# Kernel tuning notes

Hardware: AMD Instinct MI355X
Metric: run time of the kernel (lower is better)

Reference implementation:

```python
import jax, jax.numpy as jnp
import numpy as np

B, N, D, H = 8, 1025, 768, 12
PRE = 1            # prefix (CLS) tokens
P = N - PRE        # patch tokens
HD = D // H
EPS = 1e-6


def setup_inputs() -> dict:
    key = jax.random.key(0)
    ks = jax.random.split(key, 8)
    x = jax.random.normal(ks[0], (B, N, D), dtype=jnp.float32)
    graph = jax.random.uniform(ks[1], (B, P, P), dtype=jnp.float32)
    transferability = jax.random.uniform(ks[2], (B, P), dtype=jnp.float32)
    Wqkv = jax.random.normal(ks[3], (3 * D, D), dtype=jnp.float32) * 0.02
    bqkv = jnp.zeros((3 * D,), dtype=jnp.float32)
    Wproj = jax.random.normal(ks[4], (D, D), dtype=jnp.float32) * 0.02
    bproj = jnp.zeros((D,), dtype=jnp.float32)
    return {"x": x, "graph": graph, "transferability": transferability,
            "Wqkv": Wqkv, "bqkv": bqkv, "Wproj": Wproj, "bproj": bproj,
            "prefix_tokens": PRE}


def _build_mask(graph, transferability, prefix_tokens, n_tokens):
    # patch_weights: [B, P]
    pw = transferability / (jnp.sum(transferability, axis=1, keepdims=True) + EPS)
    b, p = pw.shape
    pre = prefix_tokens
    # Block layout: [[1s (pre,pre), pw broadcast (pre,P)], [pw[:,None] (P,pre), graph]]
    top_left = jnp.ones((b, pre, pre), dtype=graph.dtype)
    top_right = jnp.broadcast_to(pw[:, None, :], (b, pre, p))
    bot_left = jnp.broadcast_to(pw[:, :, None], (b, p, pre))
    top = jnp.concatenate([top_left, top_right], axis=2)
    bot = jnp.concatenate([bot_left, graph], axis=2)
    return jnp.concatenate([top, bot], axis=1)  # [B, N, N]


def reference(x, graph, transferability, Wqkv, bqkv, Wproj, bproj, prefix_tokens):
    bsz, n, d = x.shape
    scale = HD ** -0.5
    qkv = x @ Wqkv.T + bqkv                          # [B, N, 3D]
    qkv = qkv.reshape(bsz, n, 3, H, HD).transpose(2, 0, 3, 1, 4)  # [3, B, H, N, hd]
    q, k, v = qkv[0], qkv[1], qkv[2]
    attn = jax.nn.softmax(jnp.einsum('bhid,bhjd->bhij', q, k) * scale, axis=-1)
    mask = _build_mask(graph, transferability, prefix_tokens, n)  # [B, N, N]
    attn = attn * mask[:, None, :, :]
    attn = attn / (jnp.sum(attn, axis=-1, keepdims=True) + EPS)
    out = jnp.einsum('bhij,bhjd->bhid', attn, v)     # [B, H, N, hd]
    out = out.transpose(0, 2, 1, 3).reshape(bsz, n, d)
    return out @ Wproj.T + bproj
```

## Files before the change

kernel.cpp:

```cpp
#include <hip/hip_runtime.h>
#include <stdint.h>

constexpr int Bq = 8, Nn = 1025, Dd = 768, Hh = 12, HDd = 64, Pp = 1024;
constexpr int NP = 1088;
constexpr int MROWS = Bq * Nn;
constexpr float EPSI = 1e-6f;

typedef __attribute__((ext_vector_type(8))) short bfrag;
typedef __attribute__((ext_vector_type(4))) float ffrag;
typedef __attribute__((ext_vector_type(4))) float f4;
typedef __attribute__((ext_vector_type(4))) unsigned short us4;

#define MFMA16(a, b, c) __builtin_amdgcn_mfma_f32_16x16x32_bf16((a), (b), (c), 0, 0, 0)

#if __has_builtin(__builtin_amdgcn_exp2f)
#define EXP2(x) __builtin_amdgcn_exp2f(x)
#else
#define EXP2(x) exp2f(x)
#endif

__device__ __forceinline__ unsigned short f2bf(float f) {
  union { float f; uint32_t u; } v{f};
  uint32_t u = v.u;
  return (unsigned short)((u + 0x7fffu + ((u >> 16) & 1u)) >> 16);
}
__device__ __forceinline__ float bf2f(unsigned short s) {
  union { uint32_t u; float f; } v; v.u = ((uint32_t)s) << 16; return v.f;
}
__device__ __forceinline__ uint32_t pkbf(float a, float b) {
  uint32_t r;
  asm("v_cvt_pk_bf16_f32 %0, %1, %2" : "=v"(r) : "v"(a), "v"(b));
  return r;
}

__device__ __forceinline__ void gload16(const void* g, void* l) {
  __builtin_amdgcn_global_load_lds((const __attribute__((address_space(1))) unsigned int*)g,
                                   (__attribute__((address_space(3))) unsigned int*)l, 16, 0, 0);
}

__global__ __launch_bounds__(256) void conv3_kernel(const float* __restrict__ s0, unsigned short* __restrict__ d0, int n0,
                                                    const float* __restrict__ s1, unsigned short* __restrict__ d1, int n1,
                                                    const float* __restrict__ s2, unsigned short* __restrict__ d2, int n2) {
  int idx = blockIdx.x * blockDim.x + threadIdx.x;
  int stride = gridDim.x * blockDim.x;
  int ntot = n0 + n1 + n2;
  for (int i = idx; i < ntot; i += stride) {
    const float* src; unsigned short* dst; int k;
    if (i < n0) { src = s0; dst = d0; k = i; }
    else if (i < n0 + n1) { src = s1; dst = d1; k = i - n0; }
    else { src = s2; dst = d2; k = i - n0 - n1; }
    f4 v = ((const f4*)src)[k];
    us4 o; o[0] = f2bf(v[0]); o[1] = f2bf(v[1]); o[2] = f2bf(v[2]); o[3] = f2bf(v[3]);
    ((us4*)dst)[k] = o;
  }
}

__global__ __launch_bounds__(256) void pw_kernel(const float* __restrict__ tr, float* __restrict__ pw) {
  int b = blockIdx.x;
  __shared__ float red[256];
  float s = 0.f;
  for (int j = threadIdx.x; j < Pp; j += 256) s += tr[b * Pp + j];
  red[threadIdx.x] = s; __syncthreads();
  for (int o = 128; o > 0; o >>= 1) { if (threadIdx.x < o) red[threadIdx.x] += red[threadIdx.x + o]; __syncthreads(); }
  float inv = 1.f / (red[0] + EPSI);
  for (int j = threadIdx.x; j < Pp; j += 256) pw[b * Pp + j] = tr[b * Pp + j] * inv;
}

__global__ __launch_bounds__(256) void mask_kernel(const float* __restrict__ graph,
                                                   const float* __restrict__ pw,
                                                   unsigned short* __restrict__ mask) {
  int i = blockIdx.x, b = blockIdx.y;
  unsigned short* mrow = mask + ((size_t)b * NP + i) * NP;
  if (i >= Nn) { for (int j = threadIdx.x; j < NP; j += 256) mrow[j] = 0; return; }
  if (i == 0) {
    for (int j = threadIdx.x; j < NP; j += 256) {
      float v = (j == 0) ? 1.f : (j <= Pp ? pw[b * Pp + j - 1] : 0.f);
      mrow[j] = f2bf(v);
    }
  } else {
    const float* grow = graph + ((size_t)b * Pp + (i - 1)) * Pp;
    for (int j = threadIdx.x; j < NP; j += 256) {
      float v = (j == 0) ? pw[b * Pp + i - 1] : (j <= Pp ? grow[j - 1] : 0.f);
      mrow[j] = f2bf(v);
    }
  }
}

__global__ __launch_bounds__(256) void padzero_kernel(unsigned short* __restrict__ Qo,
                                                      unsigned short* __restrict__ Ko,
                                                      unsigned short* __restrict__ Vo) {
  int bh = blockIdx.x;
  unsigned short* qp = Qo + ((size_t)bh * NP + Nn) * 64;
  unsigned short* kp = Ko + ((size_t)bh * NP + Nn) * 64;
  for (int idx = threadIdx.x; idx < (NP - Nn) * 64; idx += 256) { qp[idx] = 0; kp[idx] = 0; }
  unsigned short* vp = Vo + (size_t)bh * 64 * NP;
  for (int idx = threadIdx.x; idx < 64 * (NP - Nn); idx += 256) {
    int d = idx / (NP - Nn), j = Nn + (idx - d * (NP - Nn));
    vp[(size_t)d * NP + j] = 0;
  }
}

__device__ __forceinline__ void gemm_main(const unsigned short* __restrict__ A, int rowA0, int rowAmax,
                                          const unsigned short* __restrict__ Bw, int rowB0,
                                          uint4* lds, ffrag acc[4][4], int tid) {
  const int l = tid & 63, lm = l & 15, lg = l >> 4, w = tid >> 6, wr = w >> 1, wc = w & 1;
  const unsigned short* aS[4]; const unsigned short* bS[4];
#pragma unroll
  for (int q = 0; q < 4; q++) {
    int c = tid + 256 * q, r = c >> 3, p = c & 7, g = p ^ (r & 7);
    int ra = rowA0 + r; if (ra > rowAmax) ra = rowAmax;
    aS[q] = A + (size_t)ra * 768 + 8 * g;
    bS[q] = Bw + (size_t)(rowB0 + r) * 768 + 8 * g;
  }
  uint4* buf0 = lds;
  uint4* buf1 = lds + 2048;
#pragma unroll
  for (int q = 0; q < 4; q++) {
    gload16(aS[q], buf0 + tid + 256 * q);
    gload16(bS[q], buf0 + 1024 + tid + 256 * q);
    aS[q] += 64; bS[q] += 64;
  }
  asm volatile("s_waitcnt vmcnt(0)" ::: "memory");
  __builtin_amdgcn_sched_barrier(0);
  __builtin_amdgcn_s_barrier();
#pragma unroll 1
  for (int kt = 0; kt < 12; kt++) {
    uint4* cur = (kt & 1) ? buf1 : buf0;
    uint4* nxt = (kt & 1) ? buf0 : buf1;
    if (kt < 11) {
#pragma unroll
      for (int q = 0; q < 4; q++) {
        gload16(aS[q], nxt + tid + 256 * q);
        gload16(bS[q], nxt + 1024 + tid + 256 * q);
        aS[q] += 64; bS[q] += 64;
      }
    }
    const bfrag* LA = (const bfrag*)cur;
    const bfrag* LB = (const bfrag*)(cur + 1024);
    bfrag af[4][2], bf_[4][2];
#pragma unroll
    for (int am = 0; am < 4; am++) {
      int row = wr * 64 + am * 16 + lm;
      af[am][0] = LA[row * 8 + ((0 + lg) ^ (row & 7))];
      af[am][1] = LA[row * 8 + ((4 + lg) ^ (row & 7))];
    }
#pragma unroll
    for (int an = 0; an < 4; an++) {
      int row = wc * 64 + an * 16 + lm;
      bf_[an][0] = LB[row * 8 + ((0 + lg) ^ (row & 7))];
      bf_[an][1] = LB[row * 8 + ((4 + lg) ^ (row & 7))];
    }
#pragma unroll
    for (int am = 0; am < 4; am++)
#pragma unroll
      for (int an = 0; an < 4; an++) {
        acc[am][an] = MFMA16(af[am][0], bf_[an][0], acc[am][an]);
        acc[am][an] = MFMA16(af[am][1], bf_[an][1], acc[am][an]);
      }
    asm volatile("s_waitcnt vmcnt(0)" ::: "memory");
    __builtin_amdgcn_sched_barrier(0);
    __builtin_amdgcn_s_barrier();
  }
}

__device__ __forceinline__ int xcd_chunk_map(int orig, int nwg) {
  int qq = nwg >> 3, rr = nwg & 7;
  int xcd = orig & 7, idx = orig >> 3;
  int base = (xcd < rr) ? xcd * (qq + 1) : rr * (qq + 1) + (xcd - rr) * qq;
  return base + idx;
}

__global__ __launch_bounds__(256) void qkv_gemm_kernel(const unsigned short* __restrict__ X,
                                                       const unsigned short* __restrict__ W,
                                                       const float* __restrict__ bias,
                                                       unsigned short* __restrict__ Qo,
                                                       unsigned short* __restrict__ Ko,
                                                       unsigned short* __restrict__ Vo) {
  __shared__ uint4 lds[4096];
  int tid = threadIdx.x;
  int wg = xcd_chunk_map(blockIdx.x, 65 * 18);
  int xt = wg / 18, yt = wg - 18 * xt;
  ffrag zero4 = {0.f, 0.f, 0.f, 0.f};
  ffrag acc[4][4];
#pragma unroll
  for (int i = 0; i < 4; i++)
#pragma unroll
    for (int j = 0; j < 4; j++) acc[i][j] = zero4;
  gemm_main(X, xt * 128, MROWS - 1, W, yt * 128, lds, acc, tid);
  const int l = tid & 63, lm = l & 15, lg = l >> 4, w = tid >> 6, wr = w >> 1, wc = w & 1;
#pragma unroll
  for (int an = 0; an < 4; an++) {
    int gc = yt * 128 + wc * 64 + an * 16 + lm;
    int which = gc / 768, rr = gc - which * 768, h = rr >> 6, hd = rr & 63;
    float bv = bias[gc];
#pragma unroll
    for (int am = 0; am < 4; am++) {
      int grb = xt * 128 + wr * 64 + am * 16 + 4 * lg;
#pragma unroll
      for (int r = 0; r < 4; r++) {
        int gr = grb + r;
        if (gr >= MROWS) continue;
        int b = gr / Nn, i = gr - b * Nn;
        size_t bh = (size_t)(b * Hh + h);
        float v = acc[am][an][r] + bv;
        if (which == 0)      Qo[(bh * NP + i) * 64 + hd] = f2bf(v * 0.18033688f);
        else if (which == 1) Ko[(bh * NP + i) * 64 + hd] = f2bf(v);
        else                 Vo[(bh * 64 + hd) * NP + i] = f2bf(v);
      }
    }
  }
}

__global__ __launch_bounds__(256) void proj_gemm_kernel(const unsigned short* __restrict__ A,
                                                        const unsigned short* __restrict__ W,
                                                        const float* __restrict__ bias,
                                                        float* __restrict__ out) {
  __shared__ uint4 lds[4096];
  int tid = threadIdx.x;
  int wg = xcd_chunk_map(blockIdx.x, 65 * 6);
  int xt = wg / 6, yt = wg - 6 * xt;
  ffrag zero4 = {0.f, 0.f, 0.f, 0.f};
  ffrag acc[4][4];
#pragma unroll
  for (int i = 0; i < 4; i++)
#pragma unroll
    for (int j = 0; j < 4; j++) acc[i][j] = zero4;
  gemm_main(A, xt * 128, MROWS - 1, W, yt * 128, lds, acc, tid);
  const int l = tid & 63, lm = l & 15, lg = l >> 4, w = tid >> 6, wr = w >> 1, wc = w & 1;
#pragma unroll
  for (int an = 0; an < 4; an++) {
    int gc = yt * 128 + wc * 64 + an * 16 + lm;
    float bv = bias[gc];
#pragma unroll
    for (int am = 0; am < 4; am++) {
      int grb = xt * 128 + wr * 64 + am * 16 + 4 * lg;
#pragma unroll
      for (int r = 0; r < 4; r++) {
        int gr = grb + r;
        if (gr >= MROWS) continue;
        out[(size_t)gr * 768 + gc] = acc[am][an][r] + bv;
      }
    }
  }
}

__global__ __launch_bounds__(256) void attn_kernel(const unsigned short* __restrict__ Qg,
                                                   const unsigned short* __restrict__ Kg,
                                                   const unsigned short* __restrict__ Vg,
                                                   const unsigned short* __restrict__ Mg,
                                                   unsigned short* __restrict__ Og) {
  __shared__ uint4 smem[3072];
  int tid = threadIdx.x, w = tid >> 6, l = tid & 63, lm = l & 15, lg = l >> 4;
  int bx = blockIdx.x;
  int b = bx & 7, t5 = bx >> 3;
  int h = t5 % 12, ib = t5 / 12;
  size_t bh = (size_t)(b * Hh + h);
  const unsigned short* Qb = Qg + bh * NP * 64;
  const unsigned short* Kb = Kg + bh * NP * 64;
  const unsigned short* Vb = Vg + bh * 64 * NP;
  int i0a = ib * 128 + w * 16;
  int i0b = i0a + 64;
  int irowa = i0a + lm; if (irowa > NP - 1) irowa = NP - 1;
  int irowb = i0b + lm; if (irowb > NP - 1) irowb = NP - 1;
  const unsigned short* Mrowa = Mg + (size_t)b * NP * NP + (size_t)irowa * NP;
  const unsigned short* Mrowb = Mg + (size_t)b * NP * NP + (size_t)irowb * NP;

  bfrag qa0 = *(const bfrag*)(Qb + (size_t)irowa * 64 + 8 * lg);
  bfrag qa1 = *(const bfrag*)(Qb + (size_t)irowa * 64 + 32 + 8 * lg);
  bfrag qb0 = *(const bfrag*)(Qb + (size_t)irowb * 64 + 8 * lg);
  bfrag qb1 = *(const bfrag*)(Qb + (size_t)irowb * 64 + 32 + 8 * lg);

  ffrag zero4 = {0.f, 0.f, 0.f, 0.f};
  ffrag oaccA[4] = {zero4, zero4, zero4, zero4};
  ffrag oaccB[4] = {zero4, zero4, zero4, zero4};
  float TpA = 0.f, TpB = 0.f;

  int rS = tid >> 3, pS = tid & 7;
  int rS2 = rS + 32;
  const unsigned short* kS0 = Kb + (size_t)rS * 64 + 8 * (pS ^ (rS & 7));
  const unsigned short* kS1 = Kb + (size_t)rS2 * 64 + 8 * (pS ^ (rS2 & 7));
  const unsigned short* vS0 = Vb + (size_t)rS * NP + 8 * (pS ^ (rS & 7));
  const unsigned short* vS1 = Vb + (size_t)rS2 * NP + 8 * (pS ^ (rS2 & 7));

  char* PAbase = (char*)(smem + 2048) + w * 4096;
  char* PBbase = PAbase + 2048;

  gload16(kS0, smem + tid);
  gload16(kS1, smem + tid + 256);
  gload16(vS0, smem + 512 + tid);
  gload16(vS1, smem + 512 + tid + 256);
  asm volatile("s_waitcnt vmcnt(0)" ::: "memory");
  __builtin_amdgcn_sched_barrier(0);
  __builtin_amdgcn_s_barrier();

#pragma unroll 1
  for (int t = 0; t < 17; t++) {
    int cb = (t & 1) << 10;
    if (t < 16) {
      int nb = ((t + 1) & 1) << 10;
      size_t ko = (size_t)(t + 1) * 4096;
      int vo = (t + 1) * 64;
      gload16(kS0 + ko, smem + nb + tid);
      gload16(kS1 + ko, smem + nb + tid + 256);
      gload16(vS0 + vo, smem + nb + 512 + tid);
      gload16(vS1 + vo, smem + nb + 512 + tid + 256);
    }
    int j0 = t * 64;
    us4 mvA[4], mvB[4];
#pragma unroll
    for (int jm = 0; jm < 4; jm++) {
      mvA[jm] = *(const us4*)(Mrowa + j0 + 16 * jm + 4 * lg);
      mvB[jm] = *(const us4*)(Mrowb + j0 + 16 * jm + 4 * lg);
    }
    const bfrag* LK = (const bfrag*)(smem + cb);
    const bfrag* LV = (const bfrag*)(smem + cb + 512);

    bfrag ka[4], kb2[4];
#pragma unroll
    for (int jm = 0; jm < 4; jm++) {
      int row = jm * 16 + lm;
      ka[jm]  = LK[row * 8 + ((0 + lg) ^ (row & 7))];
      kb2[jm] = LK[row * 8 + ((4 + lg) ^ (row & 7))];
    }
    ffrag sa[4], sb[4];
    __builtin_amdgcn_s_setprio(1);
#pragma unroll
    for (int jm = 0; jm < 4; jm++) {
      ffrag a = zero4;
      a = MFMA16(ka[jm], qa0, a);
      a = MFMA16(kb2[jm], qa1, a);
      sa[jm] = a;
      ffrag bb = zero4;
      bb = MFMA16(ka[jm], qb0, bb);
      bb = MFMA16(kb2[jm], qb1, bb);
      sb[jm] = bb;
    }
    __builtin_amdgcn_s_setprio(0);

    bfrag vf[2][4];
#pragma unroll
    for (int ks = 0; ks < 2; ks++)
#pragma unroll
      for (int dm = 0; dm < 4; dm++) {
        int vrow = dm * 16 + lm;
        vf[ks][dm] = LV[vrow * 8 + ((ks * 4 + lg) ^ (vrow & 7))];
      }

#pragma unroll
    for (int jm = 0; jm < 4; jm++) {
      float p0 = EXP2(sa[jm][0]), p1 = EXP2(sa[jm][1]), p2 = EXP2(sa[jm][2]), p3 = EXP2(sa[jm][3]);
      float q0 = p0 * bf2f(mvA[jm][0]), q1 = p1 * bf2f(mvA[jm][1]);
      float q2 = p2 * bf2f(mvA[jm][2]), q3 = p3 * bf2f(mvA[jm][3]);
      TpA += (q0 + q1) + (q2 + q3);
      uint2 pk; pk.x = pkbf(q0, q1); pk.y = pkbf(q2, q3);
      int cpos = (((jm << 1) | (lg >> 1)) ^ (lm & 7));
      *(uint2*)(PAbase + lm * 128 + cpos * 16 + 8 * (lg & 1)) = pk;
    }
#pragma unroll
    for (int jm = 0; jm < 4; jm++) {
      float p0 = EXP2(sb[jm][0]), p1 = EXP2(sb[jm][1]), p2 = EXP2(sb[jm][2]), p3 = EXP2(sb[jm][3]);
      float q0 = p0 * bf2f(mvB[jm][0]), q1 = p1 * bf2f(mvB[jm][1]);
      float q2 = p2 * bf2f(mvB[jm][2]), q3 = p3 * bf2f(mvB[jm][3]);
      TpB += (q0 + q1) + (q2 + q3);
      uint2 pk; pk.x = pkbf(q0, q1); pk.y = pkbf(q2, q3);
      int cpos = (((jm << 1) | (lg >> 1)) ^ (lm & 7));
      *(uint2*)(PBbase + lm * 128 + cpos * 16 + 8 * (lg & 1)) = pk;
    }
    __builtin_amdgcn_s_setprio(1);
#pragma unroll
    for (int ks = 0; ks < 2; ks++) {
      bfrag pa = *(const bfrag*)(PAbase + lm * 128 + ((((ks << 2) | lg)) ^ (lm & 7)) * 16);
#pragma unroll
      for (int dm = 0; dm < 4; dm++) oaccA[dm] = MFMA16(pa, vf[ks][dm], oaccA[dm]);
    }
#pragma unroll
    for (int ks = 0; ks < 2; ks++) {
      bfrag pb = *(const bfrag*)(PBbase + lm * 128 + ((((ks << 2) | lg)) ^ (lm & 7)) * 16);
#pragma unroll
      for (int dm = 0; dm < 4; dm++) oaccB[dm] = MFMA16(pb, vf[ks][dm], oaccB[dm]);
    }
    __builtin_amdgcn_s_setprio(0);

    asm volatile("s_waitcnt vmcnt(0)" ::: "memory");
    __builtin_amdgcn_sched_barrier(0);
    __builtin_amdgcn_s_barrier();
  }
  TpA += __shfl_xor(TpA, 16); TpA += __shfl_xor(TpA, 32);
  TpB += __shfl_xor(TpB, 16); TpB += __shfl_xor(TpB, 32);
  float dnA_row = 1.f / TpA;
  float dnB_row = 1.f / TpB;
  float dnA[4], dnB[4];
#pragma unroll
  for (int r = 0; r < 4; r++) { dnA[r] = __shfl(dnA_row, 4 * lg + r); dnB[r] = __shfl(dnB_row, 4 * lg + r); }
#pragma unroll
  for (int dm = 0; dm < 4; dm++)
#pragma unroll
    for (int r = 0; r < 4; r++) {
      int ia = i0a + 4 * lg + r;
      if (ia < Nn) Og[((size_t)(b * Nn + ia)) * Dd + h * 64 + dm * 16 + lm] = f2bf(oaccA[dm][r] * dnA[r]);
      int ibr = i0b + 4 * lg + r;
      if (ibr < Nn) Og[((size_t)(b * Nn + ibr)) * Dd + h * 64 + dm * 16 + lm] = f2bf(oaccB[dm][r] * dnB[r]);
    }
}

extern "C" void kernel_launch(void* const* d_in, const int* in_sizes, int n_in,
                              void* d_out, int out_size, void* d_ws, size_t ws_size,
                              hipStream_t stream) {
  const float* x      = (const float*)d_in[0];
  const float* graph  = (const float*)d_in[1];
  const float* transf = (const float*)d_in[2];
  const float* Wqkv   = (const float*)d_in[3];
  const float* bqkv   = (const float*)d_in[4];
  const float* Wproj  = (const float*)d_in[5];
  const float* bproj  = (const float*)d_in[6];
  float* out = (float*)d_out;
  char* ws = (char*)d_ws;

  unsigned short* xbf  = (unsigned short*)(ws + 0);
  unsigned short* wqb  = (unsigned short*)(ws + 12595200);
  unsigned short* wpb  = (unsigned short*)(ws + 16134144);
  unsigned short* Qb   = (unsigned short*)(ws + 17313792);
  unsigned short* Kb   = (unsigned short*)(ws + 30683136);
  unsigned short* Vb   = (unsigned short*)(ws + 44052480);
  float*          pw   = (float*)(ws + 57421824);
  unsigned short* mask = (unsigned short*)(ws + 57454592);
  unsigned short* aob  = xbf;

  conv3_kernel<<<2048, 256, 0, stream>>>(x, xbf, (MROWS * Dd) / 4,
                                         Wqkv, wqb, (3 * Dd * Dd) / 4,
                                         Wproj, wpb, (Dd * Dd) / 4);
  pw_kernel<<<Bq, 256, 0, stream>>>(transf, pw);
  mask_kernel<<<dim3(NP, Bq), 256, 0, stream>>>(graph, pw, mask);
  padzero_kernel<<<96, 256, 0, stream>>>(Qb, Kb, Vb);
  qkv_gemm_kernel<<<65 * 18, 256, 0, stream>>>(xbf, wqb, bqkv, Qb, Kb, Vb);
  attn_kernel<<<864, 256, 0, stream>>>(Qb, Kb, Vb, mask, aob);
  proj_gemm_kernel<<<65 * 6, 256, 0, stream>>>(aob, wpb, bproj, out);
}
```

Measured before the change: 205.4 us.

## Keep P tile in registers via 16x16x16 MFMA, drop LDS round-trip

Result: faster. 199.3 us (-2.9%).

```diff
diff --git a/kernel.cpp b/kernel.cpp
--- a/kernel.cpp
+++ b/kernel.cpp
@@ -7,11 +7,21 @@
 constexpr float EPSI = 1e-6f;
 
 typedef __attribute__((ext_vector_type(8))) short bfrag;
+typedef __attribute__((ext_vector_type(4))) short bfrag4;
 typedef __attribute__((ext_vector_type(4))) float ffrag;
 typedef __attribute__((ext_vector_type(4))) float f4;
 typedef __attribute__((ext_vector_type(4))) unsigned short us4;
 
 #define MFMA16(a, b, c) __builtin_amdgcn_mfma_f32_16x16x32_bf16((a), (b), (c), 0, 0, 0)
+
+__device__ __forceinline__ ffrag MFMA16K16(bfrag4 a, bfrag4 b, ffrag c) {
+#if __has_builtin(__builtin_amdgcn_mfma_f32_16x16x16bf16_1k)
+  return __builtin_amdgcn_mfma_f32_16x16x16bf16_1k(a, b, c, 0, 0, 0);
+#else
+  asm volatile("v_mfma_f32_16x16x16_bf16 %0, %1, %2, %0" : "+v"(c) : "v"(a), "v"(b));
+  return c;
+#endif
+}
 
 #if __has_builtin(__builtin_amdgcn_exp2f)
 #define EXP2(x) __builtin_amdgcn_exp2f(x)
@@ -70,20 +80,21 @@
                                                    const float* __restrict__ pw,
                                                    unsigned short* __restrict__ mask) {
   int i = blockIdx.x, b = blockIdx.y;
+  int t = threadIdx.x;
   unsigned short* mrow = mask + ((size_t)b * NP + i) * NP;
-  if (i >= Nn) { for (int j = threadIdx.x; j < NP; j += 256) mrow[j] = 0; return; }
-  if (i == 0) {
-    for (int j = threadIdx.x; j < NP; j += 256) {
-      float v = (j == 0) ? 1.f : (j <= Pp ? pw[b * Pp + j - 1] : 0.f);
-      mrow[j] = f2bf(v);
-    }
-  } else {
-    const float* grow = graph + ((size_t)b * Pp + (i - 1)) * Pp;
-    for (int j = threadIdx.x; j < NP; j += 256) {
-      float v = (j == 0) ? pw[b * Pp + i - 1] : (j <= Pp ? grow[j - 1] : 0.f);
-      mrow[j] = f2bf(v);
-    }
-  }
+  if (i >= Nn) {
+    for (int j = t; j < NP; j += 256) mrow[j] = 0;
+    return;
+  }
+  const float* src = (i == 0) ? (pw + b * Pp) : (graph + ((size_t)b * Pp + (i - 1)) * Pp);
+  f4 v = ((const f4*)src)[t];
+  int j = 1 + 4 * t;
+  mrow[j]     = f2bf(v[0]);
+  mrow[j + 1] = f2bf(v[1]);
+  mrow[j + 2] = f2bf(v[2]);
+  mrow[j + 3] = f2bf(v[3]);
+  if (t == 0) mrow[0] = (i == 0) ? f2bf(1.f) : f2bf(pw[b * Pp + i - 1]);
+  for (int jj = Nn + t; jj < NP; jj += 256) mrow[jj] = 0;
 }
 
 __global__ __launch_bounds__(256) void padzero_kernel(unsigned short* __restrict__ Qo,
@@ -249,7 +260,7 @@
                                                    const unsigned short* __restrict__ Vg,
                                                    const unsigned short* __restrict__ Mg,
                                                    unsigned short* __restrict__ Og) {
-  __shared__ uint4 smem[3072];
+  __shared__ uint4 smem[2048];
   int tid = threadIdx.x, w = tid >> 6, l = tid & 63, lm = l & 15, lg = l >> 4;
   int bx = blockIdx.x;
   int b = bx & 7, t5 = bx >> 3;
@@ -282,9 +293,6 @@
   const unsigned short* vS0 = Vb + (size_t)rS * NP + 8 * (pS ^ (rS & 7));
   const unsigned short* vS1 = Vb + (size_t)rS2 * NP + 8 * (pS ^ (rS2 & 7));
 
-  char* PAbase = (char*)(smem + 2048) + w * 4096;
-  char* PBbase = PAbase + 2048;
-
   gload16(kS0, smem + tid);
   gload16(kS1, smem + tid + 256);
   gload16(vS0, smem + 512 + tid);
@@ -296,6 +304,14 @@
 #pragma unroll 1
   for (int t = 0; t < 17; t++) {
     int cb = (t & 1) << 10;
+    int j0 = t * 64;
+    us4 mvA[4], mvB[4];
+#pragma unroll
+    for (int jm = 0; jm < 4; jm++) {
+      mvA[jm] = *(const us4*)(Mrowa + j0 + 16 * jm + 4 * lg);
+      mvB[jm] = *(const us4*)(Mrowb + j0 + 16 * jm + 4 * lg);
+    }
+    __builtin_amdgcn_sched_barrier(0);
     if (t < 16) {
       int nb = ((t + 1) & 1) << 10;
       size_t ko = (size_t)(t + 1) * 4096;
@@ -305,15 +321,9 @@
       gload16(vS0 + vo, smem + nb + 512 + tid);
       gload16(vS1 + vo, smem + nb + 512 + tid + 256);
     }
-    int j0 = t * 64;
-    us4 mvA[4], mvB[4];
-#pragma unroll
-    for (int jm = 0; jm < 4; jm++) {
-      mvA[jm] = *(const us4*)(Mrowa + j0 + 16 * jm + 4 * lg);
-      mvB[jm] = *(const us4*)(Mrowb + j0 + 16 * jm + 4 * lg);
-    }
+    __builtin_amdgcn_sched_barrier(0);
     const bfrag* LK = (const bfrag*)(smem + cb);
-    const bfrag* LV = (const bfrag*)(smem + cb + 512);
+    const char*  LVc = (const char*)(smem + cb + 512);
 
     bfrag ka[4], kb2[4];
 #pragma unroll
@@ -337,24 +347,28 @@
     }
     __builtin_amdgcn_s_setprio(0);
 
-    bfrag vf[2][4];
-#pragma unroll
-    for (int ks = 0; ks < 2; ks++)
+    bfrag4 vf[4][4];
+#pragma unroll
+    for (int jm = 0; jm < 4; jm++)
 #pragma unroll
       for (int dm = 0; dm < 4; dm++) {
         int vrow = dm * 16 + lm;
-        vf[ks][dm] = LV[vrow * 8 + ((ks * 4 + lg) ^ (vrow & 7))];
-      }
-
+        union { uint2 u; bfrag4 b; } cu;
+        cu.u = *(const uint2*)(LVc + vrow * 128 +
+                               ((((jm << 1) | (lg >> 1)) ^ (vrow & 7)) << 4) + 8 * (lg & 1));
+        vf[jm][dm] = cu.b;
+      }
+
+    bfrag4 paA[4], paB[4];
 #pragma unroll
     for (int jm = 0; jm < 4; jm++) {
       float p0 = EXP2(sa[jm][0]), p1 = EXP2(sa[jm][1]), p2 = EXP2(sa[jm][2]), p3 = EXP2(sa[jm][3]);
       float q0 = p0 * bf2f(mvA[jm][0]), q1 = p1 * bf2f(mvA[jm][1]);
       float q2 = p2 * bf2f(mvA[jm][2]), q3 = p3 * bf2f(mvA[jm][3]);
       TpA += (q0 + q1) + (q2 + q3);
-      uint2 pk; pk.x = pkbf(q0, q1); pk.y = pkbf(q2, q3);
-      int cpos = (((jm << 1) | (lg >> 1)) ^ (lm & 7));
-      *(uint2*)(PAbase + lm * 128 + cpos * 16 + 8 * (lg & 1)) = pk;
+      union { uint2 u; bfrag4 b; } cv;
+      cv.u.x = pkbf(q0, q1); cv.u.y = pkbf(q2, q3);
+      paA[jm] = cv.b;
     }
 #pragma unroll
     for (int jm = 0; jm < 4; jm++) {
@@ -362,23 +376,19 @@
       float q0 = p0 * bf2f(mvB[jm][0]), q1 = p1 * bf2f(mvB[jm][1]);
       float q2 = p2 * bf2f(mvB[jm][2]), q3 = p3 * bf2f(mvB[jm][3]);
       TpB += (q0 + q1) + (q2 + q3);
-      uint2 pk; pk.x = pkbf(q0, q1); pk.y = pkbf(q2, q3);
-      int cpos = (((jm << 1) | (lg >> 1)) ^ (lm & 7));
-      *(uint2*)(PBbase + lm * 128 + cpos * 16 + 8 * (lg & 1)) = pk;
-    }
+      union { uint2 u; bfrag4 b; } cv;
+      cv.u.x = pkbf(q0, q1); cv.u.y = pkbf(q2, q3);
+      paB[jm] = cv.b;
+    }
+
     __builtin_amdgcn_s_setprio(1);
 #pragma unroll
-    for (int ks = 0; ks < 2; ks++) {
-      bfrag pa = *(const bfrag*)(PAbase + lm * 128 + ((((ks << 2) | lg)) ^ (lm & 7)) * 16);
-#pragma unroll
-      for (int dm = 0; dm < 4; dm++) oaccA[dm] = MFMA16(pa, vf[ks][dm], oaccA[dm]);
-    }
-#pragma unroll
-    for (int ks = 0; ks < 2; ks++) {
-      bfrag pb = *(const bfrag*)(PBbase + lm * 128 + ((((ks << 2) | lg)) ^ (lm & 7)) * 16);
-#pragma unroll
-      for (int dm = 0; dm < 4; dm++) oaccB[dm] = MFMA16(pb, vf[ks][dm], oaccB[dm]);
-    }
+    for (int jm = 0; jm < 4; jm++)
+#pragma unroll
+      for (int dm = 0; dm < 4; dm++) {
+        oaccA[dm] = MFMA16K16(paA[jm], vf[jm][dm], oaccA[dm]);
+        oaccB[dm] = MFMA16K16(paB[jm], vf[jm][dm], oaccB[dm]);
+      }
     __builtin_amdgcn_s_setprio(0);
 
     asm volatile("s_waitcnt vmcnt(0)" ::: "memory");
```
